# Kernel tuning notes

Hardware: AMD Instinct MI355X
Metric: run time of the kernel (lower is better)

## Reference

```python
import jax, jax.numpy as jnp
import numpy as np

EMBED_DIM = 128
NUM_HEADS = 4
HEAD_DIM = EMBED_DIM // NUM_HEADS


def setup_inputs() -> dict:
    key = jax.random.key(0)
    ks = jax.random.split(key, 9)
    B, C, H, W = 8, EMBED_DIM, 64, 64
    s = 1.0 / np.sqrt(EMBED_DIM)
    x = jax.random.normal(ks[0], (B, C, H, W), dtype=jnp.float32)
    Wq = jax.random.uniform(ks[1], (EMBED_DIM, EMBED_DIM), jnp.float32, -s, s)
    bq = jax.random.uniform(ks[2], (EMBED_DIM,), jnp.float32, -s, s)
    Wk = jax.random.uniform(ks[3], (EMBED_DIM, EMBED_DIM), jnp.float32, -s, s)
    bk = jax.random.uniform(ks[4], (EMBED_DIM,), jnp.float32, -s, s)
    Wv = jax.random.uniform(ks[5], (EMBED_DIM, EMBED_DIM), jnp.float32, -s, s)
    bv = jax.random.uniform(ks[6], (EMBED_DIM,), jnp.float32, -s, s)
    Wo = jax.random.uniform(ks[7], (EMBED_DIM, EMBED_DIM), jnp.float32, -s, s)
    bo = jax.random.uniform(ks[8], (EMBED_DIM,), jnp.float32, -s, s)
    return {"x": x, "Wq": Wq, "bq": bq, "Wk": Wk, "bk": bk,
            "Wv": Wv, "bv": bv, "Wo": Wo, "bo": bo}


def reference(x, Wq, bq, Wk, bk, Wv, bv, Wo, bo):
    B, C, H, W = x.shape
    N = H * W
    # (B, C, H, W) -> (B, N, C) tokens
    t = x.reshape(B, C, N).transpose(0, 2, 1)
    # torch Linear: y = t @ W.T + b
    Q = t @ Wq.T + bq
    K = t @ Wk.T + bk
    V = t @ Wv.T + bv
    # split heads: (B, heads, N, head_dim)
    Q = Q.reshape(B, N, NUM_HEADS, HEAD_DIM).transpose(0, 2, 1, 3)
    K = K.reshape(B, N, NUM_HEADS, HEAD_DIM).transpose(0, 2, 1, 3)
    V = V.reshape(B, N, NUM_HEADS, HEAD_DIM).transpose(0, 2, 1, 3)
    scale = 1.0 / np.sqrt(HEAD_DIM).astype(np.float32)
    attn = jnp.einsum('bhnd,bhmd->bhnm', Q, K) * scale  # (B,h,N,N)
    attn = jax.nn.softmax(attn, axis=-1)
    out = jnp.einsum('bhnm,bhmd->bhnd', attn, V)
    out = out.transpose(0, 2, 1, 3).reshape(B, N, EMBED_DIM)
    out = out @ Wo.T + bo
    return out.transpose(0, 2, 1).reshape(B, EMBED_DIM, H, W)
```

## Files before the change

### kernel.cpp

```cpp
#include <hip/hip_runtime.h>


using f32x4  = __attribute__((ext_vector_type(4))) float;
using bf16x8 = __attribute__((ext_vector_type(8))) short;
using bfv8   = __attribute__((ext_vector_type(8))) __bf16;

#define QSCALE 0.17677669529663687f
#define LOG2E  1.4426950408889634f
#define QKS    (QSCALE * LOG2E)

static __device__ __forceinline__ unsigned short f2bf(float f) {
    union { float f; unsigned int u; } v; v.f = f;
    unsigned int r = v.u + 0x7FFFu + ((v.u >> 16) & 1u);
    return (unsigned short)(r >> 16);
}

static __device__ __forceinline__ f32x4 mfma16(bf16x8 a, bf16x8 b, f32x4 c) {
    return __builtin_amdgcn_mfma_f32_16x16x32_bf16(a, b, c, 0, 0, 0);
}

__global__ __launch_bounds__(256) void k_prep(
    const float* __restrict__ x,
    const float* __restrict__ Wq, const float* __restrict__ Wk,
    const float* __restrict__ Wv, const float* __restrict__ Wo,
    unsigned short* __restrict__ t_bf, unsigned short* __restrict__ Wb)
{
    const int bx = blockIdx.x;
    const int tid = threadIdx.x;
    if (bx >= 1024) {
        const int m = bx - 1024;
        const float* W = (m == 0) ? Wq : (m == 1) ? Wk : (m == 2) ? Wv : Wo;
        const float s = (m == 0) ? QKS : 1.0f;
        for (int idx = tid; idx < 16384; idx += 256)
            Wb[m * 16384 + idx] = f2bf(W[idx] * s);
        return;
    }
    __shared__ float tl[64][65];
    const int b  = bx >> 7;
    const int c0 = ((bx >> 6) & 1) * 64;
    const int n0 = (bx & 63) * 64;
    for (int idx = tid; idx < 4096; idx += 256) {
        const int ci = idx >> 6, nj = idx & 63;
        tl[ci][nj] = x[((size_t)(b * 128 + c0 + ci)) * 4096 + n0 + nj];
    }
    __syncthreads();
    for (int idx = tid; idx < 4096; idx += 256) {
        const int nj = idx >> 6, ci = idx & 63;
        t_bf[((size_t)(b * 4096 + n0 + nj)) * 128 + c0 + ci] = f2bf(tl[ci][nj]);
    }
}

__global__ __launch_bounds__(256) void k_proj3(
    const unsigned short* __restrict__ t_bf, const unsigned short* __restrict__ Wb,
    const float* __restrict__ bq, const float* __restrict__ bk, const float* __restrict__ bv,
    unsigned short* __restrict__ Qb, unsigned short* __restrict__ Kb,
    unsigned short* __restrict__ Vt)
{
    const int mat  = blockIdx.y;
    const int widx = threadIdx.x >> 6;
    const int lane = threadIdx.x & 63;
    const int g = lane >> 4, l15 = lane & 15;
    const int row0 = blockIdx.x * 64 + widx * 16;
    const int gt_row = row0 + l15;
    const unsigned short* Wm = Wb + mat * 16384;
    const float* bias = (mat == 0) ? bq : (mat == 1) ? bk : bv;

    bf16x8 tf[4];
    #pragma unroll
    for (int kc = 0; kc < 4; ++kc)
        tf[kc] = *(const bf16x8*)(t_bf + (size_t)gt_row * 128 + kc * 32 + g * 8);

    #pragma unroll
    for (int ot = 0; ot < 8; ++ot) {
        f32x4 acc;
        if (mat < 2) {
            float bb = bias[ot * 16 + l15];
            if (mat == 0) bb *= QKS;
            acc[0] = bb; acc[1] = bb; acc[2] = bb; acc[3] = bb;
        } else {
            #pragma unroll
            for (int r = 0; r < 4; ++r) acc[r] = bias[ot * 16 + 4 * g + r];
        }
        #pragma unroll
        for (int kc = 0; kc < 4; ++kc) {
            bf16x8 wf = *(const bf16x8*)(Wm + (size_t)(ot * 16 + l15) * 128 + kc * 32 + g * 8);
            acc = (mat == 2) ? mfma16(wf, tf[kc], acc) : mfma16(tf[kc], wf, acc);
        }
        if (mat < 2) {
            unsigned short* dst = (mat == 0) ? Qb : Kb;
            const int o = ot * 16 + l15, h = o >> 5, d = o & 31;
            #pragma unroll
            for (int r = 0; r < 4; ++r) {
                const int gt = row0 + 4 * g + r;
                const int b = gt >> 12, n = gt & 4095;
                dst[(((size_t)(b * 4 + h)) * 4096 + n) * 32 + d] = f2bf(acc[r]);
            }
        } else {
            const int b = gt_row >> 12, n = gt_row & 4095;
            const int n31 = n & 31;
            const int pos = ((n31 >> 2) & 3) * 8 + ((n31 >> 4) & 1) * 4 + (n31 & 3);
            #pragma unroll
            for (int r = 0; r < 4; ++r) {
                const int o = ot * 16 + 4 * g + r, h2 = o >> 5, d = o & 31;
                const size_t tb2 = ((size_t)(b * 4 + h2) * 128 + ((n >> 5) & 127)) * 1024;
                Vt[tb2 + d * 32 + pos] = f2bf(acc[r]);
            }
        }
    }
}

__global__ __launch_bounds__(256) void k_attn(
    const unsigned short* __restrict__ Qb, const unsigned short* __restrict__ Kb,
    const unsigned short* __restrict__ Vt, unsigned short* __restrict__ Ob)
{
    const int bid = blockIdx.x;
    const int swz = (bid & 7) * 256 + (bid >> 3);
    const int widx = threadIdx.x >> 6;
    const int bh = swz >> 6, q0 = (swz & 63) * 64;
    const int lane = threadIdx.x & 63, g = lane >> 4, l15 = lane & 15;

    __shared__ float lacc[3][32][68];
    __shared__ float lden[3][64];

    bf16x8 qf[4];
    #pragma unroll
    for (int f = 0; f < 4; ++f)
        qf[f] = *(const bf16x8*)(Qb + ((size_t)bh * 4096 + q0 + f * 16 + l15) * 32 + g * 8);

    const unsigned short* kp = Kb + (size_t)bh * 131072
                             + (size_t)(widx * 1024 + l15) * 32 + g * 8;
    const unsigned short* vp = Vt + (size_t)bh * 131072 + (size_t)widx * 32768
                             + l15 * 32 + g * 8;

    bf16x8 onesf;
    #pragma unroll
    for (int j = 0; j < 8; ++j) onesf[j] = (short)0x3F80;

    f32x4 aO[4][2];
    f32x4 aD[4];
    #pragma unroll
    for (int f = 0; f < 4; ++f) {
        aO[f][0] = f32x4{0.f,0.f,0.f,0.f};
        aO[f][1] = f32x4{0.f,0.f,0.f,0.f};
        aD[f]    = f32x4{0.f,0.f,0.f,0.f};
    }
    const f32x4 z = {0.f,0.f,0.f,0.f};

    for (int it = 0; it < 32; ++it) {
        const bf16x8 kf0 = *(const bf16x8*)(kp);
        const bf16x8 kf1 = *(const bf16x8*)(kp + 512);
        const bf16x8 vf0 = *(const bf16x8*)(vp);
        const bf16x8 vf1 = *(const bf16x8*)(vp + 512);
        kp += 1024;
        vp += 1024;

        #pragma unroll
        for (int f = 0; f < 4; ++f) {
            const f32x4 s0 = mfma16(kf0, qf[f], z);
            const f32x4 s1 = mfma16(kf1, qf[f], z);
            bfv8 pb;
            #pragma unroll
            for (int i = 0; i < 4; ++i) {
                pb[i]     = (__bf16)__builtin_amdgcn_exp2f(s0[i]);
                pb[4 + i] = (__bf16)__builtin_amdgcn_exp2f(s1[i]);
            }
            const bf16x8 pa = __builtin_bit_cast(bf16x8, pb);
            aO[f][0] = mfma16(pa, vf0, aO[f][0]);
            aO[f][1] = mfma16(pa, vf1, aO[f][1]);
            aD[f]    = mfma16(pa, onesf, aD[f]);
        }
    }

    if (widx != 0) {
        const int s = widx - 1;
        #pragma unroll
        for (int f = 0; f < 4; ++f) {
            *(f32x4*)&lacc[s][l15][f * 16 + 4 * g]      = aO[f][0];
            *(f32x4*)&lacc[s][16 + l15][f * 16 + 4 * g] = aO[f][1];
            if (l15 == 0) {
                #pragma unroll
                for (int r = 0; r < 4; ++r)
                    lden[s][f * 16 + 4 * g + r] = aD[f][r];
            }
        }
    }
    __syncthreads();
    if (widx != 0) return;

    const int b = bh >> 2, h = bh & 3;
    #pragma unroll
    for (int f = 0; f < 4; ++f) {
        #pragma unroll
        for (int r = 0; r < 4; ++r) {
            const int row = f * 16 + 4 * g + r;
            const float rd = 1.0f / (aD[f][r] + lden[0][row] + lden[1][row] + lden[2][row]);
            const float o0 = aO[f][0][r] + lacc[0][l15][row]
                           + lacc[1][l15][row] + lacc[2][l15][row];
            const float o1 = aO[f][1][r] + lacc[0][16 + l15][row]
                           + lacc[1][16 + l15][row] + lacc[2][16 + l15][row];
            const size_t base = ((size_t)b * 4096 + q0 + row) * 128 + h * 32;
            Ob[base + l15]      = f2bf(o0 * rd);
            Ob[base + 16 + l15] = f2bf(o1 * rd);
        }
    }
}

__global__ __launch_bounds__(256) void k_projo(
    const unsigned short* __restrict__ Ob, const unsigned short* __restrict__ Wob,
    const float* __restrict__ bo, float* __restrict__ out)
{
    const int widx = threadIdx.x >> 6;
    const int lane = threadIdx.x & 63, g = lane >> 4, l15 = lane & 15;
    const int gt = blockIdx.x * 64 + widx * 16 + l15;
    const int b = gt >> 12, n = gt & 4095;

    bf16x8 of[4];
    #pragma unroll
    for (int kc = 0; kc < 4; ++kc)
        of[kc] = *(const bf16x8*)(Ob + (size_t)gt * 128 + kc * 32 + g * 8);

    #pragma unroll
    for (int ot = 0; ot < 8; ++ot) {
        f32x4 acc;
        #pragma unroll
        for (int r = 0; r < 4; ++r) acc[r] = bo[ot * 16 + 4 * g + r];
        #pragma unroll
        for (int kc = 0; kc < 4; ++kc) {
            bf16x8 wf = *(const bf16x8*)(Wob + (size_t)(ot * 16 + l15) * 128 + kc * 32 + g * 8);
            acc = mfma16(wf, of[kc], acc);
        }
        #pragma unroll
        for (int r = 0; r < 4; ++r)
            out[((size_t)b * 128 + ot * 16 + 4 * g + r) * 4096 + n] = acc[r];
    }
}

extern "C" void kernel_launch(void* const* d_in, const int* in_sizes, int n_in,
                              void* d_out, int out_size, void* d_ws, size_t ws_size,
                              hipStream_t stream)
{
    const float* x  = (const float*)d_in[0];
    const float* Wq = (const float*)d_in[1];
    const float* bq = (const float*)d_in[2];
    const float* Wk = (const float*)d_in[3];
    const float* bk = (const float*)d_in[4];
    const float* Wv = (const float*)d_in[5];
    const float* bv = (const float*)d_in[6];
    const float* Wo = (const float*)d_in[7];
    const float* bo = (const float*)d_in[8];
    float* out = (float*)d_out;

    char* ws = (char*)d_ws;
    unsigned short* t_bf = (unsigned short*)(ws);
    unsigned short* Wb   = (unsigned short*)(ws +  8388608);
    unsigned short* Qb   = (unsigned short*)(ws +  8519680);
    unsigned short* Kb   = (unsigned short*)(ws + 16908288);
    unsigned short* Vt   = (unsigned short*)(ws + 25296896);
    unsigned short* Ob   = (unsigned short*)(ws + 33685504);

    k_prep <<<dim3(1028),     dim3(256), 0, stream>>>(x, Wq, Wk, Wv, Wo, t_bf, Wb);
    k_proj3<<<dim3(512, 3),   dim3(256), 0, stream>>>(t_bf, Wb, bq, bk, bv, Qb, Kb, Vt);
    k_attn <<<dim3(2048),     dim3(256), 0, stream>>>(Qb, Kb, Vt, Ob);
    k_projo<<<dim3(512),      dim3(256), 0, stream>>>(Ob, Wb + 3 * 16384, bo, out);
}
```

Measured before the change: 173.9 us.

## Fuse input transpose/bf16 conversion into QKV projection via shared-memory staging

Removes the intermediate t_bf buffer by having the QKV kernel load x directly, convert it to bf16 and transpose it into LDS, then run all three projections (Q, K, V) in one block instead of one grid dimension per matrix. Weight conversion moves into a tiny separate 4-block kernel. This cuts an 8 MB global write/read round trip and reads the token tile once for all three matrices, at the cost of fewer blocks (512 vs 1536) and per-block serial work over three matrices. The LDS transpose writes are 2-byte scattered stores that may bank-conflict.

```diff
diff --git a/kernel.cpp b/kernel.cpp
--- a/kernel.cpp
+++ b/kernel.cpp
@@ -19,91 +19,91 @@
     return __builtin_amdgcn_mfma_f32_16x16x32_bf16(a, b, c, 0, 0, 0);
 }
 
-__global__ __launch_bounds__(256) void k_prep(
-    const float* __restrict__ x,
+__global__ __launch_bounds__(256) void k_wprep(
     const float* __restrict__ Wq, const float* __restrict__ Wk,
     const float* __restrict__ Wv, const float* __restrict__ Wo,
-    unsigned short* __restrict__ t_bf, unsigned short* __restrict__ Wb)
-{
-    const int bx = blockIdx.x;
-    const int tid = threadIdx.x;
-    if (bx >= 1024) {
-        const int m = bx - 1024;
-        const float* W = (m == 0) ? Wq : (m == 1) ? Wk : (m == 2) ? Wv : Wo;
-        const float s = (m == 0) ? QKS : 1.0f;
-        for (int idx = tid; idx < 16384; idx += 256)
-            Wb[m * 16384 + idx] = f2bf(W[idx] * s);
-        return;
-    }
-    __shared__ float tl[64][65];
-    const int b  = bx >> 7;
-    const int c0 = ((bx >> 6) & 1) * 64;
-    const int n0 = (bx & 63) * 64;
-    for (int idx = tid; idx < 4096; idx += 256) {
-        const int ci = idx >> 6, nj = idx & 63;
-        tl[ci][nj] = x[((size_t)(b * 128 + c0 + ci)) * 4096 + n0 + nj];
-    }
-    __syncthreads();
-    for (int idx = tid; idx < 4096; idx += 256) {
-        const int nj = idx >> 6, ci = idx & 63;
-        t_bf[((size_t)(b * 4096 + n0 + nj)) * 128 + c0 + ci] = f2bf(tl[ci][nj]);
-    }
-}
-
-__global__ __launch_bounds__(256) void k_proj3(
-    const unsigned short* __restrict__ t_bf, const unsigned short* __restrict__ Wb,
+    unsigned short* __restrict__ Wb)
+{
+    const int m = blockIdx.x;
+    const float* W = (m == 0) ? Wq : (m == 1) ? Wk : (m == 2) ? Wv : Wo;
+    const float s = (m == 0) ? QKS : 1.0f;
+    for (int idx = threadIdx.x; idx < 16384; idx += 256)
+        Wb[m * 16384 + idx] = f2bf(W[idx] * s);
+}
+
+__global__ __launch_bounds__(256) void k_qkv(
+    const float* __restrict__ x, const unsigned short* __restrict__ Wb,
     const float* __restrict__ bq, const float* __restrict__ bk, const float* __restrict__ bv,
     unsigned short* __restrict__ Qb, unsigned short* __restrict__ Kb,
     unsigned short* __restrict__ Vt)
 {
-    const int mat  = blockIdx.y;
-    const int widx = threadIdx.x >> 6;
-    const int lane = threadIdx.x & 63;
-    const int g = lane >> 4, l15 = lane & 15;
-    const int row0 = blockIdx.x * 64 + widx * 16;
+    __shared__ unsigned short tl[64][136];
+    const int tid = threadIdx.x;
+    const int gt0 = blockIdx.x * 64;
+    const int b = gt0 >> 12, n0 = gt0 & 4095;
+
+    const float* xb = x + (size_t)b * 128 * 4096 + n0;
+    #pragma unroll
+    for (int k = 0; k < 8; ++k) {
+        const int flat = k * 1024 + tid * 4;
+        const int c = flat >> 6, j = flat & 63;
+        const float4 v = *(const float4*)(xb + (size_t)c * 4096 + j);
+        tl[j + 0][c] = f2bf(v.x);
+        tl[j + 1][c] = f2bf(v.y);
+        tl[j + 2][c] = f2bf(v.z);
+        tl[j + 3][c] = f2bf(v.w);
+    }
+    __syncthreads();
+
+    const int widx = tid >> 6;
+    const int lane = tid & 63, g = lane >> 4, l15 = lane & 15;
+    const int row0 = gt0 + widx * 16;
     const int gt_row = row0 + l15;
-    const unsigned short* Wm = Wb + mat * 16384;
-    const float* bias = (mat == 0) ? bq : (mat == 1) ? bk : bv;
 
     bf16x8 tf[4];
     #pragma unroll
     for (int kc = 0; kc < 4; ++kc)
-        tf[kc] = *(const bf16x8*)(t_bf + (size_t)gt_row * 128 + kc * 32 + g * 8);
-
-    #pragma unroll
-    for (int ot = 0; ot < 8; ++ot) {
-        f32x4 acc;
-        if (mat < 2) {
-            float bb = bias[ot * 16 + l15];
-            if (mat == 0) bb *= QKS;
-            acc[0] = bb; acc[1] = bb; acc[2] = bb; acc[3] = bb;
-        } else {
+        tf[kc] = *(const bf16x8*)&tl[widx * 16 + l15][kc * 32 + g * 8];
+
+    for (int mat = 0; mat < 3; ++mat) {
+        const unsigned short* Wm = Wb + mat * 16384;
+        const float* bias = (mat == 0) ? bq : (mat == 1) ? bk : bv;
+
+        #pragma unroll
+        for (int ot = 0; ot < 8; ++ot) {
+            f32x4 acc;
+            if (mat < 2) {
+                float bb = bias[ot * 16 + l15];
+                if (mat == 0) bb *= QKS;
+                acc[0] = bb; acc[1] = bb; acc[2] = bb; acc[3] = bb;
+            } else {
+                #pragma unroll
+                for (int r = 0; r < 4; ++r) acc[r] = bias[ot * 16 + 4 * g + r];
+            }
             #pragma unroll
-            for (int r = 0; r < 4; ++r) acc[r] = bias[ot * 16 + 4 * g + r];
-        }
-        #pragma unroll
-        for (int kc = 0; kc < 4; ++kc) {
-            bf16x8 wf = *(const bf16x8*)(Wm + (size_t)(ot * 16 + l15) * 128 + kc * 32 + g * 8);
-            acc = (mat == 2) ? mfma16(wf, tf[kc], acc) : mfma16(tf[kc], wf, acc);
-        }
-        if (mat < 2) {
-            unsigned short* dst = (mat == 0) ? Qb : Kb;
-            const int o = ot * 16 + l15, h = o >> 5, d = o & 31;
-            #pragma unroll
-            for (int r = 0; r < 4; ++r) {
-                const int gt = row0 + 4 * g + r;
-                const int b = gt >> 12, n = gt & 4095;
-                dst[(((size_t)(b * 4 + h)) * 4096 + n) * 32 + d] = f2bf(acc[r]);
-            }
-        } else {
-            const int b = gt_row >> 12, n = gt_row & 4095;
-            const int n31 = n & 31;
-            const int pos = ((n31 >> 2) & 3) * 8 + ((n31 >> 4) & 1) * 4 + (n31 & 3);
-            #pragma unroll
-            for (int r = 0; r < 4; ++r) {
-                const int o = ot * 16 + 4 * g + r, h2 = o >> 5, d = o & 31;
-                const size_t tb2 = ((size_t)(b * 4 + h2) * 128 + ((n >> 5) & 127)) * 1024;
-                Vt[tb2 + d * 32 + pos] = f2bf(acc[r]);
+            for (int kc = 0; kc < 4; ++kc) {
+                bf16x8 wf = *(const bf16x8*)(Wm + (size_t)(ot * 16 + l15) * 128 + kc * 32 + g * 8);
+                acc = (mat == 2) ? mfma16(wf, tf[kc], acc) : mfma16(tf[kc], wf, acc);
+            }
+            if (mat < 2) {
+                unsigned short* dst = (mat == 0) ? Qb : Kb;
+                const int o = ot * 16 + l15, h = o >> 5, d = o & 31;
+                #pragma unroll
+                for (int r = 0; r < 4; ++r) {
+                    const int gt = row0 + 4 * g + r;
+                    const int bb2 = gt >> 12, n = gt & 4095;
+                    dst[(((size_t)(bb2 * 4 + h)) * 4096 + n) * 32 + d] = f2bf(acc[r]);
+                }
+            } else {
+                const int n = gt_row & 4095;
+                const int n31 = n & 31;
+                const int pos = ((n31 >> 2) & 3) * 8 + ((n31 >> 4) & 1) * 4 + (n31 & 3);
+                #pragma unroll
+                for (int r = 0; r < 4; ++r) {
+                    const int o = ot * 16 + 4 * g + r, h2 = o >> 5, d = o & 31;
+                    const size_t tb2 = ((size_t)(b * 4 + h2) * 128 + ((n >> 5) & 127)) * 1024;
+                    Vt[tb2 + d * 32 + pos] = f2bf(acc[r]);
+                }
             }
         }
     }
@@ -251,15 +251,14 @@
     float* out = (float*)d_out;
 
     char* ws = (char*)d_ws;
-    unsigned short* t_bf = (unsigned short*)(ws);
     unsigned short* Wb   = (unsigned short*)(ws +  8388608);
     unsigned short* Qb   = (unsigned short*)(ws +  8519680);
     unsigned short* Kb   = (unsigned short*)(ws + 16908288);
     unsigned short* Vt   = (unsigned short*)(ws + 25296896);
     unsigned short* Ob   = (unsigned short*)(ws + 33685504);
 
-    k_prep <<<dim3(1028),     dim3(256), 0, stream>>>(x, Wq, Wk, Wv, Wo, t_bf, Wb);
-    k_proj3<<<dim3(512, 3),   dim3(256), 0, stream>>>(t_bf, Wb, bq, bk, bv, Qb, Kb, Vt);
-    k_attn <<<dim3(2048),     dim3(256), 0, stream>>>(Qb, Kb, Vt, Ob);
-    k_projo<<<dim3(512),      dim3(256), 0, stream>>>(Ob, Wb + 3 * 16384, bo, out);
-}
+    k_wprep<<<dim3(4),    dim3(256), 0, stream>>>(Wq, Wk, Wv, Wo, Wb);
+    k_qkv  <<<dim3(512),  dim3(256), 0, stream>>>(x, Wb, bq, bk, bv, Qb, Kb, Vt);
+    k_attn <<<dim3(2048), dim3(256), 0, stream>>>(Qb, Kb, Vt, Ob);
+    k_projo<<<dim3(512),  dim3(256), 0, stream>>>(Ob, Wb + 3 * 16384, bo, out);
+}
```

Result: no change. 173.8 us (median of 2 runs) (-0.0%).
